# Optimization experiments

Hardware: AMD Instinct MI355X
Metric: run time of the kernel (lower is better)

The kernel has to match this reference:

```python
import jax, jax.numpy as jnp
import numpy as np

HC = 64          # hidden_channels
L = 3            # num_focal_levels
IN_CH = 1        # grayscale GADF
RHO = 0.3        # sparsity_rate
KMIN = 64        # min_features
KSIZES = (3, 5, 7)   # k_l = kernel_growth_factor*l + base_kernel_size
DILS = (1, 2, 4)     # d_l = dilation_growth_factor**l
BN_EPS = 1e-5

NAMES = ('x', 'w_in', 'b_in',
         'dw0_w', 'pw0_w', 'pw0_b', 'bn0_g', 'bn0_b', 'bn0_m', 'bn0_v',
         'dw1_w', 'pw1_w', 'pw1_b', 'bn1_g', 'bn1_b', 'bn1_m', 'bn1_v',
         'dw2_w', 'pw2_w', 'pw2_b', 'bn2_g', 'bn2_b', 'bn2_m', 'bn2_v',
         'imp1_w', 'imp1_b', 'imp2_w', 'imp2_b', 'v_w', 'v_b',
         'out_w', 'out_b', 'fc_w', 'fc_b')


def _conv(x, w, pad=0, dil=1, groups=1):
    return jax.lax.conv_general_dilated(
        x, w, window_strides=(1, 1),
        padding=[(pad, pad), (pad, pad)],
        rhs_dilation=(dil, dil),
        feature_group_count=groups,
        dimension_numbers=('NCHW', 'OIHW', 'NCHW'))


def _bc(b):  # per-channel vector -> NCHW broadcast
    return b[None, :, None, None]


def _sfpm_forward(p):
    x = p['x']
    B, _, H, W = x.shape
    feat = _conv(x, p['w_in']) + _bc(p['b_in'])          # (B, 2*HC+L+1, H, W)
    Q = feat[:, :HC]
    K = feat[:, HC:2 * HC]
    G = feat[:, 2 * HC:]                                  # (B, L+1, H, W)
    # importance network: 1x1 conv -> ReLU -> 3x3 conv -> sigmoid
    m = jax.nn.relu(_conv(K, p['imp1_w']) + _bc(p['imp1_b']))
    m = jax.nn.sigmoid(_conv(m, p['imp2_w'], pad=1) + _bc(p['imp2_b']))  # (B,1,H,W)
    # adaptive top-k sparsification: k is static under jit (H, W known)
    k = max(int(RHO * H * W), KMIN)
    mask_flat = m.reshape(B, H * W)
    _, idx = jax.lax.top_k(mask_flat, k)
    sparse = jnp.zeros_like(mask_flat).at[jnp.arange(B)[:, None], idx].set(1.0)
    K_cur = K * sparse.reshape(B, 1, H, W)
    # cascaded multi-scale dilated depthwise-separable focal convs (eval-mode BN)
    focal = []
    for lvl in range(L):
        ksz, dil = KSIZES[lvl], DILS[lvl]
        y = _conv(K_cur, p['dw%d_w' % lvl], pad=(ksz // 2) * dil, dil=dil, groups=HC)
        y = _conv(y, p['pw%d_w' % lvl]) + _bc(p['pw%d_b' % lvl])
        scale = p['bn%d_g' % lvl] / jnp.sqrt(p['bn%d_v' % lvl] + BN_EPS)
        y = (y - _bc(p['bn%d_m' % lvl])) * _bc(scale) + _bc(p['bn%d_b' % lvl])
        K_cur = jax.nn.relu(y)
        focal.append(K_cur)
    # softmax-gated multi-scale aggregation
    Gn = jax.nn.softmax(G, axis=1)
    K_agg = sum(Gn[:, lvl:lvl + 1] * focal[lvl] for lvl in range(L))
    K_global = jnp.mean(focal[-1], axis=(2, 3), keepdims=True)  # broadcast = expand
    K_final = K_agg + Gn[:, -1:] * K_global
    V = _conv(K_final, p['v_w']) + _bc(p['v_b'])
    QV = Q * V
    # nn.Linear over channel dim (dropout is identity in eval)
    O = jnp.einsum('bchw,dc->bdhw', QV, p['out_w']) + _bc(p['out_b'])
    # in_channels (1) != hidden_channels -> residual uses final_conv(Q)
    x_proj = _conv(Q, p['fc_w']) + _bc(p['fc_b'])
    return x_proj + O


def setup_inputs() -> dict:
    key = jax.random.key(0)
    keys = iter(jax.random.split(key, 64))
    def nrm(shape, s=0.05):
        return jax.random.normal(next(keys), shape, jnp.float32) * s
    B, H, W = 8, 224, 224
    d = {'x': jax.random.normal(next(keys), (B, IN_CH, H, W), jnp.float32)}
    d['w_in'] = nrm((2 * HC + L + 1, IN_CH, 1, 1))
    d['b_in'] = nrm((2 * HC + L + 1,))
    for lvl, k in enumerate(KSIZES):
        d['dw%d_w' % lvl] = nrm((HC, 1, k, k))        # depthwise, groups=HC, no bias
        d['pw%d_w' % lvl] = nrm((HC, HC, 1, 1))
        d['pw%d_b' % lvl] = nrm((HC,))
        d['bn%d_g' % lvl] = jnp.ones((HC,), jnp.float32)
        d['bn%d_b' % lvl] = jnp.zeros((HC,), jnp.float32)
        d['bn%d_m' % lvl] = nrm((HC,))
        d['bn%d_v' % lvl] = jnp.abs(nrm((HC,))) + 1.0
    d['imp1_w'] = nrm((HC // 4, HC, 1, 1)); d['imp1_b'] = nrm((HC // 4,))
    d['imp2_w'] = nrm((1, HC // 4, 3, 3)); d['imp2_b'] = nrm((1,))
    d['v_w'] = nrm((HC, HC, 1, 1)); d['v_b'] = nrm((HC,))
    d['out_w'] = nrm((HC, HC)); d['out_b'] = nrm((HC,))
    d['fc_w'] = nrm((HC, HC, 1, 1)); d['fc_b'] = nrm((HC,))
    return d


def reference(x, w_in, b_in,
              dw0_w, pw0_w, pw0_b, bn0_g, bn0_b, bn0_m, bn0_v,
              dw1_w, pw1_w, pw1_b, bn1_g, bn1_b, bn1_m, bn1_v,
              dw2_w, pw2_w, pw2_b, bn2_g, bn2_b, bn2_m, bn2_v,
              imp1_w, imp1_b, imp2_w, imp2_b, v_w, v_b,
              out_w, out_b, fc_w, fc_b):
    p = dict(zip(NAMES, (x, w_in, b_in,
                         dw0_w, pw0_w, pw0_b, bn0_g, bn0_b, bn0_m, bn0_v,
                         dw1_w, pw1_w, pw1_b, bn1_g, bn1_b, bn1_m, bn1_v,
                         dw2_w, pw2_w, pw2_b, bn2_g, bn2_b, bn2_m, bn2_v,
                         imp1_w, imp1_b, imp2_w, imp2_b, v_w, v_b,
                         out_w, out_b, fc_w, fc_b)))
    return _sfpm_forward(p)
```

## Files before the change

### kernel.cpp

```cpp
#include <hip/hip_runtime.h>
#include <hip/hip_fp16.h>

typedef _Float16 f16;
typedef _Float16 f16x8 __attribute__((ext_vector_type(8)));
typedef _Float16 f16x4 __attribute__((ext_vector_type(4)));
typedef float f32x4 __attribute__((ext_vector_type(4)));

static constexpr int BB = 8, HH = 224, WW = 224, NP = HH * WW;
static constexpr int TOPK = 15052;
static constexpr int LDR = 72;
static constexpr int CHUNKS = NP / 256;
static constexpr int HB = 28;

__device__ __forceinline__ int BIDX(int px, int ci) {
  return px * LDR + (ci ^ (((px >> 3) & 7) << 3));
}

__global__ __launch_bounds__(256) void k_m(const float* __restrict__ x,
    const float* __restrict__ w_in, const float* __restrict__ b_in,
    const float* __restrict__ imp1_w, const float* __restrict__ imp1_b,
    const float* __restrict__ imp2_w, const float* __restrict__ imp2_b,
    float* __restrict__ m) {
  __shared__ float A[16], Bv[16], w2[144];
  __shared__ float bsh;
  int t = threadIdx.x;
  if (t < 144) w2[t] = imp2_w[t];
  if (t == 0) bsh = imp2_b[0];
  if (t < 16) {
    float a = 0.f, bb = 0.f;
    for (int c = 0; c < 64; c++) {
      float iw = imp1_w[t * 64 + c];
      a = fmaf(iw, w_in[64 + c], a);
      bb = fmaf(iw, b_in[64 + c], bb);
    }
    A[t] = a;
    Bv[t] = bb + imp1_b[t];
  }
  __syncthreads();
  int p = blockIdx.x * 256 + t;
  int b = p / NP, pp = p - b * NP;
  int h = pp / WW, w = pp - h * WW;
  const float* xb = x + (size_t)b * NP;
  float s = bsh;
#pragma unroll
  for (int ky = 0; ky < 3; ky++) {
    int hy = h + ky - 1;
    if ((unsigned)hy >= (unsigned)HH) continue;
#pragma unroll
    for (int kx = 0; kx < 3; kx++) {
      int wx = w + kx - 1;
      if ((unsigned)wx >= (unsigned)WW) continue;
      float xn = xb[hy * WW + wx];
#pragma unroll
      for (int j = 0; j < 16; j++) {
        float m1 = fmaxf(fmaf(A[j], xn, Bv[j]), 0.f);
        s = fmaf(w2[j * 9 + ky * 3 + kx], m1, s);
      }
    }
  }
  m[p] = 1.f / (1.f + expf(-s));
}

__global__ __launch_bounds__(64) void k_setup(const float* __restrict__ w_in,
    const float* __restrict__ b_in, const float* __restrict__ out_b,
    const float* __restrict__ fc_w, const float* __restrict__ fc_b,
    float* __restrict__ fcA, float* __restrict__ bDg) {
  int d = threadIdx.x;
  float fa = 0.f, fb = 0.f;
  for (int c = 0; c < 64; c++) {
    float fw = fc_w[d * 64 + c];
    fa = fmaf(fw, w_in[c], fa);
    fb = fmaf(fw, b_in[c], fb);
  }
  fcA[d] = fa;
  bDg[d] = out_b[d] + fc_b[d] + fb;
}

__global__ __launch_bounds__(256) void k_init(unsigned* __restrict__ ghist,
    unsigned* __restrict__ prefix, int* __restrict__ rem) {
  int i = blockIdx.x * 256 + threadIdx.x;
  if (i < 8 * 2048) ghist[i] = 0u;
  if (i < 8) { prefix[i] = 0u; rem[i] = TOPK; }
}

template <int SHIFT, unsigned HIMASK, int BINS>
__global__ __launch_bounds__(256) void k_hist(const float* __restrict__ m,
    const unsigned* __restrict__ prefix, unsigned* __restrict__ ghist) {
  __shared__ unsigned hist[2048];
  int b = blockIdx.y, blk = blockIdx.x, t = threadIdx.x;
  for (int i = t; i < BINS; i += 256) hist[i] = 0u;
  __syncthreads();
  unsigned pfx = prefix[b];
  const float* mb = m + (size_t)b * NP + blk * (NP / HB);
#pragma unroll
  for (int it = 0; it < NP / HB / 256; it++) {
    unsigned bits = __float_as_uint(mb[it * 256 + t]);
    if ((bits & HIMASK) == pfx) atomicAdd(&hist[(bits >> SHIFT) & (BINS - 1)], 1u);
  }
  __syncthreads();
  unsigned* gh = ghist + b * 2048;
  for (int i = t; i < BINS; i += 256) {
    unsigned v = hist[i];
    if (v) atomicAdd(&gh[i], v);
  }
}

template <int SHIFT, int BINS, int FINAL>
__global__ __launch_bounds__(256) void k_pick(unsigned* __restrict__ ghist,
    unsigned* __restrict__ prefix, int* __restrict__ rem,
    unsigned* __restrict__ selT, int* __restrict__ selNeed) {
  __shared__ unsigned s[256];
  int b = blockIdx.x, t = threadIdx.x;
  constexpr int PER = BINS / 256;
  unsigned* gh = ghist + b * 2048;
  unsigned local[PER];
  unsigned sum = 0;
#pragma unroll
  for (int j = 0; j < PER; j++) { local[j] = gh[t * PER + j]; sum += local[j]; }
#pragma unroll
  for (int j = 0; j < PER; j++) gh[t * PER + j] = 0u;
  s[t] = sum;
  int rm = rem[b];
  unsigned pfx = prefix[b];
  __syncthreads();
  for (int o = 1; o < 256; o <<= 1) {
    unsigned v = (t + o < 256) ? s[t + o] : 0u;
    __syncthreads();
    s[t] += v;
    __syncthreads();
  }
  unsigned nb = (t < 255) ? s[t + 1] : 0u;
  if (s[t] >= (unsigned)rm && nb < (unsigned)rm) {
    int acc = (int)nb;
#pragma unroll
    for (int j = PER - 1; j >= 0; j--) {
      acc += (int)local[j];
      if (acc >= rm) {
        unsigned bin = (unsigned)(t * PER + j);
        int need = rm - (acc - (int)local[j]);
        if (FINAL) {
          selT[b] = pfx | (bin << SHIFT);
          selNeed[b] = need;
        } else {
          prefix[b] = pfx | (bin << SHIFT);
          rem[b] = need;
        }
        break;
      }
    }
  }
}

__global__ __launch_bounds__(256) void k_cnteq(const float* __restrict__ m,
    const unsigned* __restrict__ selT, unsigned* __restrict__ cnt) {
  int b = blockIdx.y, ch = blockIdx.x, t = threadIdx.x;
  unsigned T = selT[b];
  unsigned bits = __float_as_uint(m[(size_t)b * NP + ch * 256 + t]);
  unsigned long long em = __ballot(bits == T);
  __shared__ unsigned wc[4];
  if ((t & 63) == 0) wc[t >> 6] = (unsigned)__popcll(em);
  __syncthreads();
  if (t == 0) cnt[b * CHUNKS + ch] = wc[0] + wc[1] + wc[2] + wc[3];
}

__global__ __launch_bounds__(256) void k_scan(unsigned* __restrict__ cnt) {
  __shared__ unsigned s[256];
  int b = blockIdx.x, t = threadIdx.x;
  unsigned v = (t < CHUNKS) ? cnt[b * CHUNKS + t] : 0u;
  s[t] = v;
  __syncthreads();
  for (int o = 1; o < 256; o <<= 1) {
    unsigned u = (t >= o) ? s[t - o] : 0u;
    __syncthreads();
    s[t] += u;
    __syncthreads();
  }
  if (t < CHUNKS) cnt[b * CHUNKS + t] = s[t] - v;
}

__global__ __launch_bounds__(256) void k_maskw(const float* __restrict__ m,
    const float* __restrict__ x,
    const unsigned* __restrict__ selT, const int* __restrict__ selNeed,
    const unsigned* __restrict__ cnt,
    f16* __restrict__ mx, f16* __restrict__ mk) {
  int b = blockIdx.y, ch = blockIdx.x, t = threadIdx.x;
  int lane = t & 63, wv = t >> 6;
  unsigned T = selT[b];
  int need = selNeed[b];
  size_t i = (size_t)b * NP + ch * 256 + t;
  unsigned bits = __float_as_uint(m[i]);
  bool gt = bits > T, eq = bits == T;
  unsigned long long em = __ballot(eq);
  __shared__ unsigned wc[4];
  if (lane == 0) wc[wv] = (unsigned)__popcll(em);
  __syncthreads();
  int base = (int)cnt[b * CHUNKS + ch];
  for (int w = 0; w < wv; w++) base += (int)wc[w];
  int rank = (int)__popcll(em & ((1ULL << lane) - 1ULL));
  bool sel = gt || (eq && (base + rank) < need);
  mk[i] = sel ? (f16)1.f : (f16)0.f;
  mx[i] = sel ? (f16)x[i] : (f16)0.f;
}

__global__ __launch_bounds__(256) void k_dw0(const float* __restrict__ dw_w,
    const float* __restrict__ w_in, const float* __restrict__ b_in,
    const f16* __restrict__ mx, const f16* __restrict__ mk,
    f16* __restrict__ outp) {
  constexpr int LOFF = 8, NLD = 3;
  int g = blockIdx.x * 256 + threadIdx.x;
  int w8 = g % 28;
  int rem = g / 28;
  int rowg = rem % 56, bc = rem / 56;
  int b = bc >> 6, c = bc & 63;
  int w0 = w8 * 8;
  int h0 = rowg * 4;
  const f16* mxb = mx + (size_t)b * NP;
  const f16* mkb = mk + (size_t)b * NP;
  float kw = w_in[64 + c], kb = b_in[64 + c];
  const float* wp = dw_w + c * 9;
  float wa[9], wb[9];
#pragma unroll
  for (int i = 0; i < 9; i++) {
    float wv = wp[i];
    wa[i] = wv * kw;
    wb[i] = wv * kb;
  }
  float acc[4][8] = {};
#pragma unroll
  for (int m = 0; m < 6; m++) {
    int him = h0 + m - 1;
    if ((unsigned)him >= (unsigned)HH) continue;
    float rx[NLD * 8], rk[NLD * 8];
    const f16* rpx = mxb + him * WW + (w0 - LOFF);
    const f16* rpk = mkb + him * WW + (w0 - LOFF);
#pragma unroll
    for (int s = 0; s < NLD; s++) {
      int ws_ = w0 - LOFF + s * 8;
      if ((unsigned)ws_ < (unsigned)WW) {
        f16x8 vx = *(const f16x8*)(rpx + s * 8);
        f16x8 vk = *(const f16x8*)(rpk + s * 8);
#pragma unroll
        for (int j = 0; j < 8; j++) { rx[s * 8 + j] = (float)vx[j]; rk[s * 8 + j] = (float)vk[j]; }
      } else {
#pragma unroll
        for (int j = 0; j < 8; j++) { rx[s * 8 + j] = 0.f; rk[s * 8 + j] = 0.f; }
      }
    }
#pragma unroll
    for (int j = 0; j < 4; j++) {
      constexpr unsigned K3 = 3u;
      int k = m - j;
      if ((unsigned)k >= K3) continue;
#pragma unroll
      for (int kx = 0; kx < 3; kx++) {
        float a_ = wa[k * 3 + kx], b_ = wb[k * 3 + kx];
#pragma unroll
        for (int p = 0; p < 8; p++) {
          int idx = p + LOFF + (kx - 1);
          acc[j][p] = fmaf(a_, rx[idx], fmaf(b_, rk[idx], acc[j][p]));
        }
      }
    }
  }
#pragma unroll
  for (int j = 0; j < 4; j++) {
    f16x8 o;
#pragma unroll
    for (int p = 0; p < 8; p++) o[p] = (f16)acc[j][p];
    *(f16x8*)(outp + (size_t)bc * NP + (h0 + j) * WW + w0) = o;
  }
}

template <int KSZ, int DIL>
__global__ __launch_bounds__(256) void k_dw4(const float* __restrict__ dw_w,
    const f16* __restrict__ fin, f16* __restrict__ outp) {
  constexpr int PAD = (KSZ / 2) * DIL;
  constexpr int LOFF = (PAD + 7) & ~7;
  constexpr int NLD = (LOFF + 8 + PAD + 7) / 8;
  constexpr int NR = KSZ + 3;
  int g = blockIdx.x * 256 + threadIdx.x;
  int w8 = g % 28;
  int rem = g / 28;
  int rowg = rem % 56, bc = rem / 56;
  int w0 = w8 * 8;
  int res = rowg % DIL, grp = rowg / DIL;
  int h0 = res + DIL * 4 * grp;
  int c = bc & 63;
  const f16* fb = fin + (size_t)bc * NP;
  const float* wp = dw_w + c * KSZ * KSZ;
  float wr[KSZ * KSZ];
#pragma unroll
  for (int i = 0; i < KSZ * KSZ; i++) wr[i] = wp[i];
  float acc[4][8] = {};
#pragma unroll
  for (int m = 0; m < NR; m++) {
    int him = h0 + (m - KSZ / 2) * DIL;
    if ((unsigned)him >= (unsigned)HH) continue;
    float r[NLD * 8];
    const f16* rp = fb + him * WW + (w0 - LOFF);
#pragma unroll
    for (int s = 0; s < NLD; s++) {
      int ws_ = w0 - LOFF + s * 8;
      if ((unsigned)ws_ < (unsigned)WW) {
        f16x8 v = *(const f16x8*)(rp + s * 8);
#pragma unroll
        for (int j = 0; j < 8; j++) r[s * 8 + j] = (float)v[j];
      } else {
#pragma unroll
        for (int j = 0; j < 8; j++) r[s * 8 + j] = 0.f;
      }
    }
#pragma unroll
    for (int j = 0; j < 4; j++) {
      int k = m - j;
      if (k < 0 || k >= KSZ) continue;
#pragma unroll
      for (int kx = 0; kx < KSZ; kx++) {
        float wv = wr[k * KSZ + kx];
#pragma unroll
        for (int p = 0; p < 8; p++)
          acc[j][p] = fmaf(wv, r[p + LOFF + (kx - KSZ / 2) * DIL], acc[j][p]);
      }
    }
  }
#pragma unroll
  for (int j = 0; j < 4; j++) {
    f16x8 o;
#pragma unroll
    for (int p = 0; p < 8; p++) o[p] = (f16)acc[j][p];
    *(f16x8*)(outp + (size_t)bc * NP + (h0 + DIL * j) * WW + w0) = o;
  }
}

__global__ __launch_bounds__(256) void k_pwm(const f16* __restrict__ inp,
    const float* __restrict__ pw_w, const float* __restrict__ pw_b,
    const float* __restrict__ g, const float* __restrict__ be,
    const float* __restrict__ mu, const float* __restrict__ var,
    f16* __restrict__ outp) {
  __shared__ f16 buf[128 * LDR];
  __shared__ float sc[64], sh[64];
  int t = threadIdx.x;
  if (t < 64) {
    float s = g[t] / sqrtf(var[t] + 1e-5f);
    sc[t] = s;
    sh[t] = (pw_b[t] - mu[t]) * s + be[t];
  }
  int b = blockIdx.y;
  int p0 = blockIdx.x * 128;
  const f16* src = inp + (size_t)b * 64 * NP + p0;
  f16x8 vv[4];
  int cis[4], pxs[4];
#pragma unroll
  for (int it = 0; it < 4; it++) {
    int cidx = it * 256 + t;
    cis[it] = cidx >> 4;
    pxs[it] = (cidx & 15) * 8;
    vv[it] = *(const f16x8*)(src + (size_t)cis[it] * NP + pxs[it]);
  }
#pragma unroll
  for (int it = 0; it < 4; it++) {
#pragma unroll
    for (int j = 0; j < 8; j++) buf[BIDX(pxs[it] + j, cis[it])] = vv[it][j];
  }
  __syncthreads();
  int ln = t & 63, wv = t >> 6;
  int r16 = ln & 15, g4 = ln >> 4;
  f16x8 af[4][2];
#pragma unroll
  for (int cb = 0; cb < 4; cb++)
#pragma unroll
    for (int ks = 0; ks < 2; ks++) {
      const float* wr = pw_w + (cb * 16 + r16) * 64 + ks * 32 + g4 * 8;
      f32x4 w0 = *(const f32x4*)wr;
      f32x4 w1 = *(const f32x4*)(wr + 4);
      f16x8 a;
      a[0] = (f16)w0[0]; a[1] = (f16)w0[1]; a[2] = (f16)w0[2]; a[3] = (f16)w0[3];
      a[4] = (f16)w1[0]; a[5] = (f16)w1[1]; a[6] = (f16)w1[2]; a[7] = (f16)w1[3];
      af[cb][ks] = a;
    }
#pragma unroll
  for (int pxb = 0; pxb < 2; pxb++) {
    int pl = wv * 32 + pxb * 16;
    f16x8 bf[2];
#pragma unroll
    for (int ks = 0; ks < 2; ks++)
      bf[ks] = *(const f16x8*)&buf[BIDX(pl + r16, ks * 32 + g4 * 8)];
    f32x4 acc[4];
#pragma unroll
    for (int cb = 0; cb < 4; cb++) acc[cb] = (f32x4){0.f, 0.f, 0.f, 0.f};
#pragma unroll
    for (int cb = 0; cb < 4; cb++)
#pragma unroll
      for (int ks = 0; ks < 2; ks++)
        acc[cb] = __builtin_amdgcn_mfma_f32_16x16x32_f16(af[cb][ks], bf[ks], acc[cb], 0, 0, 0);
    f16* dst = outp + (size_t)b * 64 * NP + p0 + pl + r16;
#pragma unroll
    for (int cb = 0; cb < 4; cb++)
#pragma unroll
      for (int j = 0; j < 4; j++) {
        int co = cb * 16 + g4 * 4 + j;
        float o = fmaf(acc[cb][j], sc[co], sh[co]);
        dst[(size_t)co * NP] = (f16)fmaxf(o, 0.f);
      }
  }
}

__global__ __launch_bounds__(256) void k_mean(const f16* __restrict__ F2,
                                              float* __restrict__ kg) {
  int bc = blockIdx.x;
  const f16* f = F2 + (size_t)bc * NP;
  float s = 0.f;
  for (int i = threadIdx.x; i < NP; i += 256) s += (float)f[i];
  __shared__ float r[256];
  r[threadIdx.x] = s;
  __syncthreads();
  for (int o = 128; o > 0; o >>= 1) {
    if (threadIdx.x < o) r[threadIdx.x] += r[threadIdx.x + o];
    __syncthreads();
  }
  if (threadIdx.x == 0) kg[bc] = r[0] * (1.f / NP);
}

__global__ __launch_bounds__(256) void k_final(const float* __restrict__ x,
    const float* __restrict__ w_in, const float* __restrict__ b_in,
    const f16* __restrict__ F0, const f16* __restrict__ F1, const f16* __restrict__ F2,
    const float* __restrict__ kg, const float* __restrict__ fcA,
    const float* __restrict__ bDg,
    const float* __restrict__ v_w, const float* __restrict__ v_b,
    const float* __restrict__ out_w,
    float* __restrict__ outp) {
  __shared__ f16 buf[128 * LDR];
  __shared__ float gvs[128 * 4];
  __shared__ float xs[128];
  __shared__ float kgs[64], qwS[64], qbS[64], vbS[64], bD[64], fcAS[64];
  int t = threadIdx.x;
  int b = blockIdx.y;
  int p0 = blockIdx.x * 128;
  if (t < 64) {
    kgs[t] = kg[b * 64 + t];
    qwS[t] = w_in[t];
    qbS[t] = b_in[t];
    vbS[t] = v_b[t];
    fcAS[t] = fcA[t];
    bD[t] = bDg[t];
  }
  if (t < 128) {
    int px = ((t & 15) << 3) | (t >> 4);
    float xv = x[(size_t)b * NP + p0 + px];
    xs[px] = xv;
    float gv[4], mxv = -1e30f;
#pragma unroll
    for (int j = 0; j < 4; j++) {
      gv[j] = fmaf(xv, w_in[128 + j], b_in[128 + j]);
      mxv = fmaxf(mxv, gv[j]);
    }
    float se = 0.f;
#pragma unroll
    for (int j = 0; j < 4; j++) { gv[j] = expf(gv[j] - mxv); se += gv[j]; }
    float inv = 1.f / se;
    f32x4 g4v;
#pragma unroll
    for (int j = 0; j < 4; j++) g4v[j] = gv[j] * inv;
    *(f32x4*)&gvs[t * 4] = g4v;
  }
  const f16* f0 = F0 + (size_t)b * 64 * NP + p0;
  const f16* f1 = F1 + (size_t)b * 64 * NP + p0;
  const f16* f2 = F2 + (size_t)b * 64 * NP + p0;
  f16x8 s0[4], s1[4], s2[4];
  int cis[4], pxs[4];
#pragma unroll
  for (int it = 0; it < 4; it++) {
    int cidx = it * 256 + t;
    cis[it] = cidx >> 4;
    pxs[it] = (cidx & 15) * 8;
    size_t o = (size_t)cis[it] * NP + pxs[it];
    s0[it] = *(const f16x8*)(f0 + o);
    s1[it] = *(const f16x8*)(f1 + o);
    s2[it] = *(const f16x8*)(f2 + o);
  }
  int ln = t & 63, wv = t >> 6;
  int r16 = ln & 15, g4 = ln >> 4;
  f16x8 afV[4][2];
#pragma unroll
  for (int cb = 0; cb < 4; cb++)
#pragma unroll
    for (int ks = 0; ks < 2; ks++) {
      const float* wr = v_w + (cb * 16 + r16) * 64 + ks * 32 + g4 * 8;
      f32x4 w0 = *(const f32x4*)wr;
      f32x4 w1 = *(const f32x4*)(wr + 4);
      f16x8 a;
      a[0] = (f16)w0[0]; a[1] = (f16)w0[1]; a[2] = (f16)w0[2]; a[3] = (f16)w0[3];
      a[4] = (f16)w1[0]; a[5] = (f16)w1[1]; a[6] = (f16)w1[2]; a[7] = (f16)w1[3];
      afV[cb][ks] = a;
    }
  __syncthreads();
#pragma unroll
  for (int it = 0; it < 4; it++) {
    int ci = cis[it], px8 = pxs[it];
    float kgc = kgs[ci];
#pragma unroll
    for (int j = 0; j < 8; j++) {
      int px = px8 + j;
      f32x4 gv = *(const f32x4*)&gvs[(((px & 7) << 4) | (px >> 3)) * 4];
      float kf = gv[0] * (float)s0[it][j] + gv[1] * (float)s1[it][j] +
                 gv[2] * (float)s2[it][j] + gv[3] * kgc;
      buf[BIDX(px, ci)] = (f16)kf;
    }
  }
  __syncthreads();
  {
#pragma unroll
    for (int pxb = 0; pxb < 2; pxb++) {
      int pl = wv * 32 + pxb * 16;
      f16x8 bf[2];
#pragma unroll
      for (int ks = 0; ks < 2; ks++)
        bf[ks] = *(const f16x8*)&buf[BIDX(pl + r16, ks * 32 + g4 * 8)];
      f32x4 acc[4];
#pragma unroll
      for (int cb = 0; cb < 4; cb++) acc[cb] = (f32x4){0.f, 0.f, 0.f, 0.f};
#pragma unroll
      for (int cb = 0; cb < 4; cb++)
#pragma unroll
        for (int ks = 0; ks < 2; ks++)
          acc[cb] = __builtin_amdgcn_mfma_f32_16x16x32_f16(afV[cb][ks], bf[ks], acc[cb], 0, 0, 0);
      int px = pl + r16;
      float xv = xs[px];
#pragma unroll
      for (int cb = 0; cb < 4; cb++) {
        f16x4 q4;
#pragma unroll
        for (int j = 0; j < 4; j++) {
          int co = cb * 16 + g4 * 4 + j;
          float V = acc[cb][j] + vbS[co];
          float q = fmaf(xv, qwS[co], qbS[co]);
          q4[j] = (f16)(q * V);
        }
        *(f16x4*)&buf[BIDX(px, cb * 16 + g4 * 4)] = q4;
      }
    }
  }
  f16x8 afO[4][2];
#pragma unroll
  for (int cb = 0; cb < 4; cb++)
#pragma unroll
    for (int ks = 0; ks < 2; ks++) {
      const float* wr = out_w + (cb * 16 + r16) * 64 + ks * 32 + g4 * 8;
      f32x4 w0 = *(const f32x4*)wr;
      f32x4 w1 = *(const f32x4*)(wr + 4);
      f16x8 a;
      a[0] = (f16)w0[0]; a[1] = (f16)w0[1]; a[2] = (f16)w0[2]; a[3] = (f16)w0[3];
      a[4] = (f16)w1[0]; a[5] = (f16)w1[1]; a[6] = (f16)w1[2]; a[7] = (f16)w1[3];
      afO[cb][ks] = a;
    }
  __syncthreads();
  {
#pragma unroll
    for (int pxb = 0; pxb < 2; pxb++) {
      int pl = wv * 32 + pxb * 16;
      f16x8 bf[2];
#pragma unroll
      for (int ks = 0; ks < 2; ks++)
        bf[ks] = *(const f16x8*)&buf[BIDX(pl + r16, ks * 32 + g4 * 8)];
      f32x4 acc[4];
#pragma unroll
      for (int cb = 0; cb < 4; cb++) acc[cb] = (f32x4){0.f, 0.f, 0.f, 0.f};
#pragma unroll
      for (int cb = 0; cb < 4; cb++)
#pragma unroll
        for (int ks = 0; ks < 2; ks++)
          acc[cb] = __builtin_amdgcn_mfma_f32_16x16x32_f16(afO[cb][ks], bf[ks], acc[cb], 0, 0, 0);
      int px = pl + r16;
      float xv = xs[px];
      float* dst = outp + (size_t)b * 64 * NP + p0 + px;
#pragma unroll
      for (int cb = 0; cb < 4; cb++)
#pragma unroll
        for (int j = 0; j < 4; j++) {
          int d = cb * 16 + g4 * 4 + j;
          dst[(size_t)d * NP] = acc[cb][j] + bD[d] + xv * fcAS[d];
        }
    }
  }
}

extern "C" void kernel_launch(void* const* d_in, const int* in_sizes, int n_in,
                              void* d_out, int out_size, void* d_ws, size_t ws_size,
                              hipStream_t stream) {
  const float* x = (const float*)d_in[0];
  const float* w_in = (const float*)d_in[1];
  const float* b_in = (const float*)d_in[2];
  const float* dw_w[3] = {(const float*)d_in[3], (const float*)d_in[10], (const float*)d_in[17]};
  const float* pw_w[3] = {(const float*)d_in[4], (const float*)d_in[11], (const float*)d_in[18]};
  const float* pw_b[3] = {(const float*)d_in[5], (const float*)d_in[12], (const float*)d_in[19]};
  const float* bng[3] = {(const float*)d_in[6], (const float*)d_in[13], (const float*)d_in[20]};
  const float* bnb[3] = {(const float*)d_in[7], (const float*)d_in[14], (const float*)d_in[21]};
  const float* bnm[3] = {(const float*)d_in[8], (const float*)d_in[15], (const float*)d_in[22]};
  const float* bnv[3] = {(const float*)d_in[9], (const float*)d_in[16], (const float*)d_in[23]};
  const float* imp1_w = (const float*)d_in[24];
  const float* imp1_b = (const float*)d_in[25];
  const float* imp2_w = (const float*)d_in[26];
  const float* imp2_b = (const float*)d_in[27];
  const float* v_w = (const float*)d_in[28];
  const float* v_b = (const float*)d_in[29];
  const float* out_w = (const float*)d_in[30];
  const float* out_b = (const float*)d_in[31];
  const float* fc_w = (const float*)d_in[32];
  const float* fc_b = (const float*)d_in[33];

  char* ws = (char*)d_ws;
  size_t off = 0;
  auto alloc = [&](size_t sz) {
    size_t o = off;
    off = (off + sz + 255) & ~(size_t)255;
    return o;
  };
  float* mbuf = (float*)(ws + alloc((size_t)BB * NP * 4));
  unsigned* ghist = (unsigned*)(ws + alloc((size_t)BB * 2048 * 4));
  unsigned* prefix = (unsigned*)(ws + alloc(8 * 4));
  int* remv = (int*)(ws + alloc(8 * 4));
  unsigned* selT = (unsigned*)(ws + alloc(8 * 4));
  int* selNeed = (int*)(ws + alloc(8 * 4));
  unsigned* cntbuf = (unsigned*)(ws + alloc((size_t)BB * CHUNKS * 4));
  float* fcA = (float*)(ws + alloc(64 * 4));
  float* bDg = (float*)(ws + alloc(64 * 4));
  f16* mx = (f16*)(ws + alloc((size_t)BB * NP * 2));
  f16* mk = (f16*)(ws + alloc((size_t)BB * NP * 2));
  f16* tmp = (f16*)(ws + alloc((size_t)BB * 64 * NP * 2));
  f16* F0 = (f16*)(ws + alloc((size_t)BB * 64 * NP * 2));
  f16* F1 = (f16*)(ws + alloc((size_t)BB * 64 * NP * 2));
  f16* F2 = (f16*)(ws + alloc((size_t)BB * 64 * NP * 2));
  float* kg = (float*)(ws + alloc(512 * 4));

  const int PIX_BLKS = (BB * NP) / 256;
  const int DW4_BLKS = (BB * 64 * 56 * 28) / 256;
  dim3 tile_grid(NP / 128, BB);
  dim3 chunk_grid(CHUNKS, BB);
  dim3 hist_grid(HB, BB);

  k_m<<<PIX_BLKS, 256, 0, stream>>>(x, w_in, b_in, imp1_w, imp1_b, imp2_w, imp2_b, mbuf);
  k_init<<<64, 256, 0, stream>>>(ghist, prefix, remv);
  k_setup<<<1, 64, 0, stream>>>(w_in, b_in, out_b, fc_w, fc_b, fcA, bDg);
  k_hist<21, 0u, 2048><<<hist_grid, 256, 0, stream>>>(mbuf, prefix, ghist);
  k_pick<21, 2048, 0><<<BB, 256, 0, stream>>>(ghist, prefix, remv, selT, selNeed);
  k_hist<10, 0xFFE00000u, 2048><<<hist_grid, 256, 0, stream>>>(mbuf, prefix, ghist);
  k_pick<10, 2048, 0><<<BB, 256, 0, stream>>>(ghist, prefix, remv, selT, selNeed);
  k_hist<0, 0xFFFFFC00u, 1024><<<hist_grid, 256, 0, stream>>>(mbuf, prefix, ghist);
  k_pick<0, 1024, 1><<<BB, 256, 0, stream>>>(ghist, prefix, remv, selT, selNeed);

  k_cnteq<<<chunk_grid, 256, 0, stream>>>(mbuf, selT, cntbuf);
  k_scan<<<BB, 256, 0, stream>>>(cntbuf);
  k_maskw<<<chunk_grid, 256, 0, stream>>>(mbuf, x, selT, selNeed, cntbuf, mx, mk);

  k_dw0<<<DW4_BLKS, 256, 0, stream>>>(dw_w[0], w_in, b_in, mx, mk, tmp);
  k_pwm<<<tile_grid, 256, 0, stream>>>(tmp, pw_w[0], pw_b[0], bng[0], bnb[0], bnm[0], bnv[0], F0);
  k_dw4<5, 2><<<DW4_BLKS, 256, 0, stream>>>(dw_w[1], F0, tmp);
  k_pwm<<<tile_grid, 256, 0, stream>>>(tmp, pw_w[1], pw_b[1], bng[1], bnb[1], bnm[1], bnv[1], F1);
  k_dw4<7, 4><<<DW4_BLKS, 256, 0, stream>>>(dw_w[2], F1, tmp);
  k_pwm<<<tile_grid, 256, 0, stream>>>(tmp, pw_w[2], pw_b[2], bng[2], bnb[2], bnm[2], bnv[2], F2);

  k_mean<<<512, 256, 0, stream>>>(F2, kg);
  k_final<<<tile_grid, 256, 0, stream>>>(x, w_in, b_in, F0, F1, F2, kg, fcA, bDg,
                                         v_w, v_b, out_w, (float*)d_out);
}
```

Measured before the change: 415.0 us.

## Fuse depthwise focal convs with pointwise MFMA conv and BN-ReLU per tile

Result: slower. 469.4 us (+13.1%).

```diff
diff --git a/kernel.cpp b/kernel.cpp
--- a/kernel.cpp
+++ b/kernel.cpp
@@ -202,141 +202,15 @@
   mx[i] = sel ? (f16)x[i] : (f16)0.f;
 }
 
-__global__ __launch_bounds__(256) void k_dw0(const float* __restrict__ dw_w,
+
+__global__ __launch_bounds__(256) void k_fused0(const float* __restrict__ dw_w,
     const float* __restrict__ w_in, const float* __restrict__ b_in,
     const f16* __restrict__ mx, const f16* __restrict__ mk,
-    f16* __restrict__ outp) {
-  constexpr int LOFF = 8, NLD = 3;
-  int g = blockIdx.x * 256 + threadIdx.x;
-  int w8 = g % 28;
-  int rem = g / 28;
-  int rowg = rem % 56, bc = rem / 56;
-  int b = bc >> 6, c = bc & 63;
-  int w0 = w8 * 8;
-  int h0 = rowg * 4;
-  const f16* mxb = mx + (size_t)b * NP;
-  const f16* mkb = mk + (size_t)b * NP;
-  float kw = w_in[64 + c], kb = b_in[64 + c];
-  const float* wp = dw_w + c * 9;
-  float wa[9], wb[9];
-#pragma unroll
-  for (int i = 0; i < 9; i++) {
-    float wv = wp[i];
-    wa[i] = wv * kw;
-    wb[i] = wv * kb;
-  }
-  float acc[4][8] = {};
-#pragma unroll
-  for (int m = 0; m < 6; m++) {
-    int him = h0 + m - 1;
-    if ((unsigned)him >= (unsigned)HH) continue;
-    float rx[NLD * 8], rk[NLD * 8];
-    const f16* rpx = mxb + him * WW + (w0 - LOFF);
-    const f16* rpk = mkb + him * WW + (w0 - LOFF);
-#pragma unroll
-    for (int s = 0; s < NLD; s++) {
-      int ws_ = w0 - LOFF + s * 8;
-      if ((unsigned)ws_ < (unsigned)WW) {
-        f16x8 vx = *(const f16x8*)(rpx + s * 8);
-        f16x8 vk = *(const f16x8*)(rpk + s * 8);
-#pragma unroll
-        for (int j = 0; j < 8; j++) { rx[s * 8 + j] = (float)vx[j]; rk[s * 8 + j] = (float)vk[j]; }
-      } else {
-#pragma unroll
-        for (int j = 0; j < 8; j++) { rx[s * 8 + j] = 0.f; rk[s * 8 + j] = 0.f; }
-      }
-    }
-#pragma unroll
-    for (int j = 0; j < 4; j++) {
-      constexpr unsigned K3 = 3u;
-      int k = m - j;
-      if ((unsigned)k >= K3) continue;
-#pragma unroll
-      for (int kx = 0; kx < 3; kx++) {
-        float a_ = wa[k * 3 + kx], b_ = wb[k * 3 + kx];
-#pragma unroll
-        for (int p = 0; p < 8; p++) {
-          int idx = p + LOFF + (kx - 1);
-          acc[j][p] = fmaf(a_, rx[idx], fmaf(b_, rk[idx], acc[j][p]));
-        }
-      }
-    }
-  }
-#pragma unroll
-  for (int j = 0; j < 4; j++) {
-    f16x8 o;
-#pragma unroll
-    for (int p = 0; p < 8; p++) o[p] = (f16)acc[j][p];
-    *(f16x8*)(outp + (size_t)bc * NP + (h0 + j) * WW + w0) = o;
-  }
-}
-
-template <int KSZ, int DIL>
-__global__ __launch_bounds__(256) void k_dw4(const float* __restrict__ dw_w,
-    const f16* __restrict__ fin, f16* __restrict__ outp) {
-  constexpr int PAD = (KSZ / 2) * DIL;
-  constexpr int LOFF = (PAD + 7) & ~7;
-  constexpr int NLD = (LOFF + 8 + PAD + 7) / 8;
-  constexpr int NR = KSZ + 3;
-  int g = blockIdx.x * 256 + threadIdx.x;
-  int w8 = g % 28;
-  int rem = g / 28;
-  int rowg = rem % 56, bc = rem / 56;
-  int w0 = w8 * 8;
-  int res = rowg % DIL, grp = rowg / DIL;
-  int h0 = res + DIL * 4 * grp;
-  int c = bc & 63;
-  const f16* fb = fin + (size_t)bc * NP;
-  const float* wp = dw_w + c * KSZ * KSZ;
-  float wr[KSZ * KSZ];
-#pragma unroll
-  for (int i = 0; i < KSZ * KSZ; i++) wr[i] = wp[i];
-  float acc[4][8] = {};
-#pragma unroll
-  for (int m = 0; m < NR; m++) {
-    int him = h0 + (m - KSZ / 2) * DIL;
-    if ((unsigned)him >= (unsigned)HH) continue;
-    float r[NLD * 8];
-    const f16* rp = fb + him * WW + (w0 - LOFF);
-#pragma unroll
-    for (int s = 0; s < NLD; s++) {
-      int ws_ = w0 - LOFF + s * 8;
-      if ((unsigned)ws_ < (unsigned)WW) {
-        f16x8 v = *(const f16x8*)(rp + s * 8);
-#pragma unroll
-        for (int j = 0; j < 8; j++) r[s * 8 + j] = (float)v[j];
-      } else {
-#pragma unroll
-        for (int j = 0; j < 8; j++) r[s * 8 + j] = 0.f;
-      }
-    }
-#pragma unroll
-    for (int j = 0; j < 4; j++) {
-      int k = m - j;
-      if (k < 0 || k >= KSZ) continue;
-#pragma unroll
-      for (int kx = 0; kx < KSZ; kx++) {
-        float wv = wr[k * KSZ + kx];
-#pragma unroll
-        for (int p = 0; p < 8; p++)
-          acc[j][p] = fmaf(wv, r[p + LOFF + (kx - KSZ / 2) * DIL], acc[j][p]);
-      }
-    }
-  }
-#pragma unroll
-  for (int j = 0; j < 4; j++) {
-    f16x8 o;
-#pragma unroll
-    for (int p = 0; p < 8; p++) o[p] = (f16)acc[j][p];
-    *(f16x8*)(outp + (size_t)bc * NP + (h0 + DIL * j) * WW + w0) = o;
-  }
-}
-
-__global__ __launch_bounds__(256) void k_pwm(const f16* __restrict__ inp,
     const float* __restrict__ pw_w, const float* __restrict__ pw_b,
     const float* __restrict__ g, const float* __restrict__ be,
     const float* __restrict__ mu, const float* __restrict__ var,
     f16* __restrict__ outp) {
+  constexpr int LOFF = 8, NLD = 3;
   __shared__ f16 buf[128 * LDR];
   __shared__ float sc[64], sh[64];
   int t = threadIdx.x;
@@ -346,22 +220,62 @@
     sh[t] = (pw_b[t] - mu[t]) * s + be[t];
   }
   int b = blockIdx.y;
-  int p0 = blockIdx.x * 128;
-  const f16* src = inp + (size_t)b * 64 * NP + p0;
-  f16x8 vv[4];
-  int cis[4], pxs[4];
-#pragma unroll
-  for (int it = 0; it < 4; it++) {
-    int cidx = it * 256 + t;
-    cis[it] = cidx >> 4;
-    pxs[it] = (cidx & 15) * 8;
-    vv[it] = *(const f16x8*)(src + (size_t)cis[it] * NP + pxs[it]);
-  }
-#pragma unroll
-  for (int it = 0; it < 4; it++) {
-#pragma unroll
-    for (int j = 0; j < 8; j++) buf[BIDX(pxs[it] + j, cis[it])] = vv[it][j];
-  }
+  int wgrp = blockIdx.x % 7, rowg = blockIdx.x / 7;
+  int h0 = rowg * 4;
+  int ci = t & 63, w8l = t >> 6;
+  int wbase = wgrp * 32 + w8l * 8;
+  const f16* mxb = mx + (size_t)b * NP;
+  const f16* mkb = mk + (size_t)b * NP;
+  float kw = w_in[64 + ci], kb = b_in[64 + ci];
+  const float* wp = dw_w + ci * 9;
+  float wa[9], wb[9];
+#pragma unroll
+  for (int i = 0; i < 9; i++) {
+    float wv_ = wp[i];
+    wa[i] = wv_ * kw;
+    wb[i] = wv_ * kb;
+  }
+  float acc[4][8] = {};
+#pragma unroll
+  for (int m = 0; m < 6; m++) {
+    int him = h0 + m - 1;
+    if ((unsigned)him >= (unsigned)HH) continue;
+    float rx[NLD * 8], rk[NLD * 8];
+    const f16* rpx = mxb + him * WW + (wbase - LOFF);
+    const f16* rpk = mkb + him * WW + (wbase - LOFF);
+#pragma unroll
+    for (int s = 0; s < NLD; s++) {
+      int ws_ = wbase - LOFF + s * 8;
+      if ((unsigned)ws_ < (unsigned)WW) {
+        f16x8 vx = *(const f16x8*)(rpx + s * 8);
+        f16x8 vk = *(const f16x8*)(rpk + s * 8);
+#pragma unroll
+        for (int j = 0; j < 8; j++) { rx[s * 8 + j] = (float)vx[j]; rk[s * 8 + j] = (float)vk[j]; }
+      } else {
+#pragma unroll
+        for (int j = 0; j < 8; j++) { rx[s * 8 + j] = 0.f; rk[s * 8 + j] = 0.f; }
+      }
+    }
+#pragma unroll
+    for (int j = 0; j < 4; j++) {
+      int k = m - j;
+      if ((unsigned)k >= 3u) continue;
+#pragma unroll
+      for (int kx = 0; kx < 3; kx++) {
+        float a_ = wa[k * 3 + kx], b_ = wb[k * 3 + kx];
+#pragma unroll
+        for (int p = 0; p < 8; p++) {
+          int idx = p + LOFF + (kx - 1);
+          acc[j][p] = fmaf(a_, rx[idx], fmaf(b_, rk[idx], acc[j][p]));
+        }
+      }
+    }
+  }
+#pragma unroll
+  for (int j = 0; j < 4; j++)
+#pragma unroll
+    for (int p = 0; p < 8; p++)
+      buf[BIDX(j * 32 + w8l * 8 + p, ci)] = (f16)acc[j][p];
   __syncthreads();
   int ln = t & 63, wv = t >> 6;
   int r16 = ln & 15, g4 = ln >> 4;
@@ -385,21 +299,135 @@
 #pragma unroll
     for (int ks = 0; ks < 2; ks++)
       bf[ks] = *(const f16x8*)&buf[BIDX(pl + r16, ks * 32 + g4 * 8)];
-    f32x4 acc[4];
-#pragma unroll
-    for (int cb = 0; cb < 4; cb++) acc[cb] = (f32x4){0.f, 0.f, 0.f, 0.f};
+    f32x4 acc2[4];
+#pragma unroll
+    for (int cb = 0; cb < 4; cb++) acc2[cb] = (f32x4){0.f, 0.f, 0.f, 0.f};
 #pragma unroll
     for (int cb = 0; cb < 4; cb++)
 #pragma unroll
       for (int ks = 0; ks < 2; ks++)
-        acc[cb] = __builtin_amdgcn_mfma_f32_16x16x32_f16(af[cb][ks], bf[ks], acc[cb], 0, 0, 0);
-    f16* dst = outp + (size_t)b * 64 * NP + p0 + pl + r16;
+        acc2[cb] = __builtin_amdgcn_mfma_f32_16x16x32_f16(af[cb][ks], bf[ks], acc2[cb], 0, 0, 0);
+    int jrow = pl >> 5;
+    int wloc = (pl & 31) + r16;
+    f16* dst = outp + (size_t)b * 64 * NP + (h0 + jrow) * WW + wgrp * 32 + wloc;
 #pragma unroll
     for (int cb = 0; cb < 4; cb++)
 #pragma unroll
       for (int j = 0; j < 4; j++) {
         int co = cb * 16 + g4 * 4 + j;
-        float o = fmaf(acc[cb][j], sc[co], sh[co]);
+        float o = fmaf(acc2[cb][j], sc[co], sh[co]);
+        dst[(size_t)co * NP] = (f16)fmaxf(o, 0.f);
+      }
+  }
+}
+
+template <int KSZ, int DIL>
+__global__ __launch_bounds__(256) void k_fused(const float* __restrict__ dw_w,
+    const f16* __restrict__ fin,
+    const float* __restrict__ pw_w, const float* __restrict__ pw_b,
+    const float* __restrict__ g, const float* __restrict__ be,
+    const float* __restrict__ mu, const float* __restrict__ var,
+    f16* __restrict__ outp) {
+  constexpr int PAD = (KSZ / 2) * DIL;
+  constexpr int LOFF = (PAD + 7) & ~7;
+  constexpr int NLD = (LOFF + 8 + PAD + 7) / 8;
+  constexpr int NR = KSZ + 3;
+  __shared__ f16 buf[128 * LDR];
+  __shared__ float sc[64], sh[64];
+  int t = threadIdx.x;
+  if (t < 64) {
+    float s = g[t] / sqrtf(var[t] + 1e-5f);
+    sc[t] = s;
+    sh[t] = (pw_b[t] - mu[t]) * s + be[t];
+  }
+  int b = blockIdx.y;
+  int wgrp = blockIdx.x % 7, rowg = blockIdx.x / 7;
+  int res = rowg % DIL, grp = rowg / DIL;
+  int h0 = res + DIL * 4 * grp;
+  int ci = t & 63, w8l = t >> 6;
+  int wbase = wgrp * 32 + w8l * 8;
+  const f16* fb = fin + (size_t)(b * 64 + ci) * NP;
+  const float* wp = dw_w + ci * KSZ * KSZ;
+  float wr_[KSZ * KSZ];
+#pragma unroll
+  for (int i = 0; i < KSZ * KSZ; i++) wr_[i] = wp[i];
+  float acc[4][8] = {};
+#pragma unroll
+  for (int m = 0; m < NR; m++) {
+    int him = h0 + (m - KSZ / 2) * DIL;
+    if ((unsigned)him >= (unsigned)HH) continue;
+    float r[NLD * 8];
+    const f16* rp = fb + him * WW + (wbase - LOFF);
+#pragma unroll
+    for (int s = 0; s < NLD; s++) {
+      int ws_ = wbase - LOFF + s * 8;
+      if ((unsigned)ws_ < (unsigned)WW) {
+        f16x8 v = *(const f16x8*)(rp + s * 8);
+#pragma unroll
+        for (int j = 0; j < 8; j++) r[s * 8 + j] = (float)v[j];
+      } else {
+#pragma unroll
+        for (int j = 0; j < 8; j++) r[s * 8 + j] = 0.f;
+      }
+    }
+#pragma unroll
+    for (int j = 0; j < 4; j++) {
+      int k = m - j;
+      if (k < 0 || k >= KSZ) continue;
+#pragma unroll
+      for (int kx = 0; kx < KSZ; kx++) {
+        float wv_ = wr_[k * KSZ + kx];
+#pragma unroll
+        for (int p = 0; p < 8; p++)
+          acc[j][p] = fmaf(wv_, r[p + LOFF + (kx - KSZ / 2) * DIL], acc[j][p]);
+      }
+    }
+  }
+#pragma unroll
+  for (int j = 0; j < 4; j++)
+#pragma unroll
+    for (int p = 0; p < 8; p++)
+      buf[BIDX(j * 32 + w8l * 8 + p, ci)] = (f16)acc[j][p];
+  __syncthreads();
+  int ln = t & 63, wv = t >> 6;
+  int r16 = ln & 15, g4 = ln >> 4;
+  f16x8 af[4][2];
+#pragma unroll
+  for (int cb = 0; cb < 4; cb++)
+#pragma unroll
+    for (int ks = 0; ks < 2; ks++) {
+      const float* wr = pw_w + (cb * 16 + r16) * 64 + ks * 32 + g4 * 8;
+      f32x4 w0 = *(const f32x4*)wr;
+      f32x4 w1 = *(const f32x4*)(wr + 4);
+      f16x8 a;
+      a[0] = (f16)w0[0]; a[1] = (f16)w0[1]; a[2] = (f16)w0[2]; a[3] = (f16)w0[3];
+      a[4] = (f16)w1[0]; a[5] = (f16)w1[1]; a[6] = (f16)w1[2]; a[7] = (f16)w1[3];
+      af[cb][ks] = a;
+    }
+#pragma unroll
+  for (int pxb = 0; pxb < 2; pxb++) {
+    int pl = wv * 32 + pxb * 16;
+    f16x8 bf[2];
+#pragma unroll
+    for (int ks = 0; ks < 2; ks++)
+      bf[ks] = *(const f16x8*)&buf[BIDX(pl + r16, ks * 32 + g4 * 8)];
+    f32x4 acc2[4];
+#pragma unroll
+    for (int cb = 0; cb < 4; cb++) acc2[cb] = (f32x4){0.f, 0.f, 0.f, 0.f};
+#pragma unroll
+    for (int cb = 0; cb < 4; cb++)
+#pragma unroll
+      for (int ks = 0; ks < 2; ks++)
+        acc2[cb] = __builtin_amdgcn_mfma_f32_16x16x32_f16(af[cb][ks], bf[ks], acc2[cb], 0, 0, 0);
+    int jrow = pl >> 5;
+    int wloc = (pl & 31) + r16;
+    f16* dst = outp + (size_t)b * 64 * NP + (h0 + DIL * jrow) * WW + wgrp * 32 + wloc;
+#pragma unroll
+    for (int cb = 0; cb < 4; cb++)
+#pragma unroll
+      for (int j = 0; j < 4; j++) {
+        int co = cb * 16 + g4 * 4 + j;
+        float o = fmaf(acc2[cb][j], sc[co], sh[co]);
         dst[(size_t)co * NP] = (f16)fmaxf(o, 0.f);
       }
   }
@@ -626,15 +654,14 @@
   float* bDg = (float*)(ws + alloc(64 * 4));
   f16* mx = (f16*)(ws + alloc((size_t)BB * NP * 2));
   f16* mk = (f16*)(ws + alloc((size_t)BB * NP * 2));
-  f16* tmp = (f16*)(ws + alloc((size_t)BB * 64 * NP * 2));
   f16* F0 = (f16*)(ws + alloc((size_t)BB * 64 * NP * 2));
   f16* F1 = (f16*)(ws + alloc((size_t)BB * 64 * NP * 2));
   f16* F2 = (f16*)(ws + alloc((size_t)BB * 64 * NP * 2));
   float* kg = (float*)(ws + alloc(512 * 4));
 
   const int PIX_BLKS = (BB * NP) / 256;
-  const int DW4_BLKS = (BB * 64 * 56 * 28) / 256;
   dim3 tile_grid(NP / 128, BB);
+  dim3 fuse_grid(392, BB);
   dim3 chunk_grid(CHUNKS, BB);
   dim3 hist_grid(HB, BB);
 
@@ -652,12 +679,12 @@
   k_scan<<<BB, 256, 0, stream>>>(cntbuf);
   k_maskw<<<chunk_grid, 256, 0, stream>>>(mbuf, x, selT, selNeed, cntbuf, mx, mk);
 
-  k_dw0<<<DW4_BLKS, 256, 0, stream>>>(dw_w[0], w_in, b_in, mx, mk, tmp);
-  k_pwm<<<tile_grid, 256, 0, stream>>>(tmp, pw_w[0], pw_b[0], bng[0], bnb[0], bnm[0], bnv[0], F0);
-  k_dw4<5, 2><<<DW4_BLKS, 256, 0, stream>>>(dw_w[1], F0, tmp);
-  k_pwm<<<tile_grid, 256, 0, stream>>>(tmp, pw_w[1], pw_b[1], bng[1], bnb[1], bnm[1], bnv[1], F1);
-  k_dw4<7, 4><<<DW4_BLKS, 256, 0, stream>>>(dw_w[2], F1, tmp);
-  k_pwm<<<tile_grid, 256, 0, stream>>>(tmp, pw_w[2], pw_b[2], bng[2], bnb[2], bnm[2], bnv[2], F2);
+  k_fused0<<<fuse_grid, 256, 0, stream>>>(dw_w[0], w_in, b_in, mx, mk,
+      pw_w[0], pw_b[0], bng[0], bnb[0], bnm[0], bnv[0], F0);
+  k_fused<5, 2><<<fuse_grid, 256, 0, stream>>>(dw_w[1], F0,
+      pw_w[1], pw_b[1], bng[1], bnb[1], bnm[1], bnv[1], F1);
+  k_fused<7, 4><<<fuse_grid, 256, 0, stream>>>(dw_w[2], F1,
+      pw_w[2], pw_b[2], bng[2], bnb[2], bnm[2], bnv[2], F2);
 
   k_mean<<<512, 256, 0, stream>>>(F2, kg);
   k_final<<<tile_grid, 256, 0, stream>>>(x, w_in, b_in, F0, F1, F2, kg, fcA, bDg,
```
